# Kernel tuning notes

Hardware: AMD Instinct MI355X
Metric: run time of the kernel (lower is better)

The kernel has to match this reference:

```python
import jax, jax.numpy as jnp
import numpy as np

B, T, D_IN, D_OUT = 8, 2048, 4096, 4096
N_ADAPTERS, R_MAX = 8, 64


def setup_inputs() -> dict:
    key = jax.random.key(0)
    k_x, k_base, k_idx, k_A, k_B, k_s = jax.random.split(key, 6)
    x = jax.random.normal(k_x, (B, T, D_IN), dtype=jnp.float32)
    base_output = jax.random.normal(k_base, (B, T, D_OUT), dtype=jnp.float32)
    adapter_indices = jax.random.randint(k_idx, (B,), 0, N_ADAPTERS, dtype=jnp.int64)
    # He-uniform init for A (kaiming_uniform with a=sqrt(5) -> bound = 1/sqrt(fan_in))
    bound = 1.0 / np.sqrt(D_IN)
    lora_A = jax.random.uniform(k_A, (N_ADAPTERS, D_IN, R_MAX), dtype=jnp.float32,
                                minval=-bound, maxval=bound)
    # lora_B is zeros at init; use small random values for a non-trivial reference
    lora_B = jax.random.normal(k_B, (N_ADAPTERS, R_MAX, D_OUT), dtype=jnp.float32) * 0.02
    lora_scaling = jax.random.uniform(k_s, (N_ADAPTERS,), dtype=jnp.float32,
                                      minval=0.5, maxval=2.0)
    return {"x": x, "base_output": base_output, "adapter_indices": adapter_indices,
            "lora_A": lora_A, "lora_B": lora_B, "lora_scaling": lora_scaling}


def reference(x, base_output, adapter_indices, lora_A, lora_B, lora_scaling):
    # Gather per-batch adapter weights (adapter index broadcasts over sequence):
    # equivalent to sort-by-adapter -> grouped GEMM -> unsort, since every token
    # in a batch row shares one adapter and all ranks equal r_max.
    A_b = lora_A[adapter_indices]          # [B, D_IN, R]
    B_b = lora_B[adapter_indices]          # [B, R, D_OUT]
    s_b = lora_scaling[adapter_indices]    # [B]
    inter = jnp.einsum('btd,bdr->btr', x, A_b)        # [B, T, R]
    y = jnp.einsum('btr,bro->bto', inter, B_b)        # [B, T, D_OUT]
    return base_output + y * s_b[:, None, None]
```

## Files before the change

### kernel.cpp

```cpp
#include <hip/hip_runtime.h>
#include <hip/hip_bf16.h>
#include <cstdint>
#include <cstddef>

#define BT    16384
#define DIN   4096
#define DOUT  4096
#define RR    64
#define TSEQ  2048
#define NADP  8

typedef float  f32x4  __attribute__((ext_vector_type(4)));
typedef __bf16 bf16x8 __attribute__((ext_vector_type(8)));

static __device__ __forceinline__ unsigned short bf16_bits(float f) {
    return __builtin_bit_cast(unsigned short, (__bf16)f);
}

static __device__ __forceinline__ size_t i2_idx(int mblk, int rb, int mrow, int j) {
    return ((((size_t)mblk * 8 + rb) * 16 + mrow) * 8 + j);
}

__global__ __launch_bounds__(256) void k_prep_a(
    const float* __restrict__ A, __bf16* __restrict__ At2)
{
    const int gtid = blockIdx.x * 256 + threadIdx.x;
    const int r  = gtid & 63;
    const int kb = (gtid >> 6) & (DIN / 8 - 1);
    const int a  = gtid >> 15;
    const float* __restrict__ src = A + (size_t)a * DIN * RR + (size_t)kb * 8 * RR + r;
    unsigned int u[4];
    #pragma unroll
    for (int p = 0; p < 4; ++p) {
        unsigned int lo = bf16_bits(src[(2 * p + 0) * RR]);
        unsigned int hi = bf16_bits(src[(2 * p + 1) * RR]);
        u[p] = lo | (hi << 16);
    }
    *(uint4*)&At2[(size_t)gtid * 8] = make_uint4(u[0], u[1], u[2], u[3]);
}

__global__ __launch_bounds__(256) void k_prep_b(
    const float* __restrict__ Bw, __bf16* __restrict__ Bp)
{
    const int gtid = blockIdx.x * 256 + threadIdx.x;
    const int o  = gtid & (DOUT - 1);
    const int rb = (gtid >> 12) & 7;
    const int a  = gtid >> 15;
    const float* __restrict__ src = Bw + (size_t)a * RR * DOUT + (size_t)rb * 8 * DOUT + o;
    unsigned int u[4];
    #pragma unroll
    for (int p = 0; p < 4; ++p) {
        unsigned int lo = bf16_bits(src[(2 * p + 0) * DOUT]);
        unsigned int hi = bf16_bits(src[(2 * p + 1) * DOUT]);
        u[p] = lo | (hi << 16);
    }
    *(uint4*)&Bp[(size_t)gtid * 8] = make_uint4(u[0], u[1], u[2], u[3]);
}

static __device__ __forceinline__ bf16x8 cvt8(float4 a, float4 b) {
    bf16x8 v;
    v[0] = (__bf16)a.x; v[1] = (__bf16)a.y; v[2] = (__bf16)a.z; v[3] = (__bf16)a.w;
    v[4] = (__bf16)b.x; v[5] = (__bf16)b.y; v[6] = (__bf16)b.z; v[7] = (__bf16)b.w;
    return v;
}

__global__ __launch_bounds__(256, 2) void k_xa(
    const float* __restrict__ x, const int* __restrict__ idx,
    const __bf16* __restrict__ At2, __bf16* __restrict__ inter2)
{
    __shared__ __bf16 xs[2][32][64];

    const int tid  = threadIdx.x;
    const int m0   = blockIdx.x * 32;
    const int a    = idx[m0 / TSEQ];
    const int w    = tid >> 6, lane = tid & 63;
    const int mr   = lane & 15, kg = lane >> 4;

    const int srow = tid >> 3;
    const int sj   = tid & 7;
    const int sk8  = sj ^ (srow & 7);
    const float* __restrict__ xsrc = x + (size_t)(m0 + srow) * DIN + sk8 * 8;
    __bf16* const xdst0 = &xs[0][srow][sj * 8];
    __bf16* const xdst1 = &xs[1][srow][sj * 8];

    const __bf16* __restrict__ Aw = At2 + (size_t)a * RR * DIN;
    const int rcol = w * 16 + mr;

    f32x4 z = {0.f, 0.f, 0.f, 0.f};
    f32x4 acc0 = z, acc1 = z;

    float4 rbA0, rbA1, rbB0, rbB1;

    rbA0 = *(const float4*)(xsrc + 0 * 64);
    rbA1 = *(const float4*)(xsrc + 0 * 64 + 4);
    rbB0 = *(const float4*)(xsrc + 1 * 64);
    rbB1 = *(const float4*)(xsrc + 1 * 64 + 4);
    *(bf16x8*)xdst0 = cvt8(rbA0, rbA1);
    __syncthreads();

    for (int t2 = 0; t2 < 32; ++t2) {
        const int t = 2 * t2;
        const int tp2 = (t + 2 <= 63) ? (t + 2) : 63;
        const int tp3 = (t + 3 <= 63) ? (t + 3) : 63;

        rbA0 = *(const float4*)(xsrc + tp2 * 64);
        rbA1 = *(const float4*)(xsrc + tp2 * 64 + 4);
        #pragma unroll
        for (int kstep = 0; kstep < 2; ++kstep) {
            const int kq = kstep * 4 + kg;
            bf16x8 bfw = *(const bf16x8*)&Aw[((size_t)(t * 8 + kq) * 64 + rcol) * 8];
            bf16x8 af0 = *(const bf16x8*)&xs[0][mr]     [(kq ^ (mr & 7)) * 8];
            bf16x8 af1 = *(const bf16x8*)&xs[0][16 + mr][(kq ^ (mr & 7)) * 8];
            acc0 = __builtin_amdgcn_mfma_f32_16x16x32_bf16(af0, bfw, acc0, 0, 0, 0);
            acc1 = __builtin_amdgcn_mfma_f32_16x16x32_bf16(af1, bfw, acc1, 0, 0, 0);
        }
        *(bf16x8*)xdst1 = cvt8(rbB0, rbB1);
        __syncthreads();

        rbB0 = *(const float4*)(xsrc + tp3 * 64);
        rbB1 = *(const float4*)(xsrc + tp3 * 64 + 4);
        #pragma unroll
        for (int kstep = 0; kstep < 2; ++kstep) {
            const int kq = kstep * 4 + kg;
            bf16x8 bfw = *(const bf16x8*)&Aw[((size_t)((t + 1) * 8 + kq) * 64 + rcol) * 8];
            bf16x8 af0 = *(const bf16x8*)&xs[1][mr]     [(kq ^ (mr & 7)) * 8];
            bf16x8 af1 = *(const bf16x8*)&xs[1][16 + mr][(kq ^ (mr & 7)) * 8];
            acc0 = __builtin_amdgcn_mfma_f32_16x16x32_bf16(af0, bfw, acc0, 0, 0, 0);
            acc1 = __builtin_amdgcn_mfma_f32_16x16x32_bf16(af1, bfw, acc1, 0, 0, 0);
        }
        *(bf16x8*)xdst0 = cvt8(rbA0, rbA1);
        __syncthreads();
    }

    const int rb = w * 2 + (mr >> 3), j = mr & 7;
    #pragma unroll
    for (int q = 0; q < 4; ++q) {
        inter2[i2_idx(blockIdx.x * 2 + 0, rb, kg * 4 + q, j)] = (__bf16)acc0[q];
        inter2[i2_idx(blockIdx.x * 2 + 1, rb, kg * 4 + q, j)] = (__bf16)acc1[q];
    }
}

__global__ __launch_bounds__(256) void k_by(
    const __bf16* __restrict__ inter2, const float* __restrict__ base,
    const int* __restrict__ idx, const __bf16* __restrict__ Bp,
    const float* __restrict__ scal, float* __restrict__ out)
{
    const int o0 = blockIdx.x * 64;
    const int m0 = blockIdx.y * 64;
    const int a  = idx[m0 / TSEQ];
    const float s = scal[a];
    const __bf16* __restrict__ Ba = Bp + (size_t)a * RR * DOUT;
    const int lane = threadIdx.x & 63;
    const int w    = threadIdx.x >> 6;
    const int mr   = lane & 15, kg = lane >> 4;
    const int oc   = o0 + w * 16 + mr;

    f32x4 z = {0.f, 0.f, 0.f, 0.f};
    f32x4 acc[4] = {z, z, z, z};

    #pragma unroll
    for (int ksub = 0; ksub < 2; ++ksub) {
        const int rb = ksub * 4 + kg;
        bf16x8 bfA = *(const bf16x8*)&Ba[((size_t)rb * DOUT + oc) * 8];
        #pragma unroll
        for (int mt = 0; mt < 4; ++mt) {
            bf16x8 afB = *(const bf16x8*)&inter2[i2_idx(m0 / 16 + mt, rb, mr, 0)];
            acc[mt] = __builtin_amdgcn_mfma_f32_16x16x32_bf16(bfA, afB, acc[mt], 0, 0, 0);
        }
    }

    #pragma unroll
    for (int mt = 0; mt < 4; ++mt) {
        size_t off = (size_t)(m0 + mt * 16 + mr) * DOUT + o0 + w * 16 + kg * 4;
        float4 bv = *(const float4*)&base[off];
        float4 o;
        o.x = bv.x + s * acc[mt][0];
        o.y = bv.y + s * acc[mt][1];
        o.z = bv.z + s * acc[mt][2];
        o.w = bv.w + s * acc[mt][3];
        *(float4*)&out[off] = o;
    }
}

__global__ __launch_bounds__(256) void k_xa_fb(
    const float* __restrict__ x, const int* __restrict__ idx,
    const float* __restrict__ A, __bf16* __restrict__ inter)
{
    const int m0   = blockIdx.x * 32;
    const int a    = idx[m0 / TSEQ];
    const float* __restrict__ Aa = A + (size_t)a * DIN * RR;
    const int lane = threadIdx.x & 63;
    const int rw   = threadIdx.x >> 6;
    const int mr   = lane & 15, kg = lane >> 4;
    const int rcol = rw * 16 + mr;
    const float* __restrict__ xrow0 = x + (size_t)(m0 + mr) * DIN;
    const float* __restrict__ xrow1 = x + (size_t)(m0 + 16 + mr) * DIN;

    f32x4 acc0 = {0.f, 0.f, 0.f, 0.f};
    f32x4 acc1 = {0.f, 0.f, 0.f, 0.f};

    for (int k0 = 0; k0 < DIN; k0 += 64) {
        #pragma unroll
        for (int ksub = 0; ksub < 2; ++ksub) {
            const int koff = k0 + ksub * 32 + kg * 8;
            float4 u0 = *(const float4*)&xrow0[koff];
            float4 u1 = *(const float4*)&xrow0[koff + 4];
            float4 v0 = *(const float4*)&xrow1[koff];
            float4 v1 = *(const float4*)&xrow1[koff + 4];
            bf16x8 af0 = cvt8(u0, u1);
            bf16x8 af1 = cvt8(v0, v1);
            const float* ap = &Aa[(size_t)koff * RR + rcol];
            bf16x8 bf;
            bf[0] = (__bf16)ap[0 * RR]; bf[1] = (__bf16)ap[1 * RR];
            bf[2] = (__bf16)ap[2 * RR]; bf[3] = (__bf16)ap[3 * RR];
            bf[4] = (__bf16)ap[4 * RR]; bf[5] = (__bf16)ap[5 * RR];
            bf[6] = (__bf16)ap[6 * RR]; bf[7] = (__bf16)ap[7 * RR];
            acc0 = __builtin_amdgcn_mfma_f32_16x16x32_bf16(af0, bf, acc0, 0, 0, 0);
            acc1 = __builtin_amdgcn_mfma_f32_16x16x32_bf16(af1, bf, acc1, 0, 0, 0);
        }
    }
    #pragma unroll
    for (int q = 0; q < 4; ++q) {
        inter[(size_t)(m0 + kg * 4 + q) * RR + rcol]      = (__bf16)acc0[q];
        inter[(size_t)(m0 + 16 + kg * 4 + q) * RR + rcol] = (__bf16)acc1[q];
    }
}

__global__ __launch_bounds__(256) void k_by_fb(
    const __bf16* __restrict__ inter, const float* __restrict__ base,
    const int* __restrict__ idx, const float* __restrict__ Bw,
    const float* __restrict__ scal, float* __restrict__ out)
{
    const int o0 = blockIdx.x * 64;
    const int m0 = blockIdx.y * 64;
    const int a  = idx[m0 / TSEQ];
    const float s = scal[a];
    const float* __restrict__ Ba = Bw + (size_t)a * RR * DOUT;
    const int lane = threadIdx.x & 63;
    const int w    = threadIdx.x >> 6;
    const int mr   = lane & 15, kg = lane >> 4;
    const int oc   = o0 + w * 16 + mr;

    f32x4 z = {0.f, 0.f, 0.f, 0.f};
    f32x4 acc[4] = {z, z, z, z};

    #pragma unroll
    for (int ksub = 0; ksub < 2; ++ksub) {
        const int kb = ksub * 32 + kg * 8;
        const float* bp = &Ba[(size_t)kb * DOUT + oc];
        bf16x8 bf;
        bf[0] = (__bf16)bp[0 * DOUT]; bf[1] = (__bf16)bp[1 * DOUT];
        bf[2] = (__bf16)bp[2 * DOUT]; bf[3] = (__bf16)bp[3 * DOUT];
        bf[4] = (__bf16)bp[4 * DOUT]; bf[5] = (__bf16)bp[5 * DOUT];
        bf[6] = (__bf16)bp[6 * DOUT]; bf[7] = (__bf16)bp[7 * DOUT];
        #pragma unroll
        for (int mt = 0; mt < 4; ++mt) {
            bf16x8 af = *(const bf16x8*)&inter[(size_t)(m0 + mt * 16 + mr) * RR + kb];
            acc[mt] = __builtin_amdgcn_mfma_f32_16x16x32_bf16(af, bf, acc[mt], 0, 0, 0);
        }
    }
    #pragma unroll
    for (int mt = 0; mt < 4; ++mt) {
        #pragma unroll
        for (int q = 0; q < 4; ++q) {
            size_t off = (size_t)(m0 + mt * 16 + kg * 4 + q) * DOUT + oc;
            out[off] = base[off] + s * acc[mt][q];
        }
    }
}

extern "C" void kernel_launch(void* const* d_in, const int* in_sizes, int n_in,
                              void* d_out, int out_size, void* d_ws, size_t ws_size,
                              hipStream_t stream)
{
    const float* x    = (const float*)d_in[0];
    const float* base = (const float*)d_in[1];
    const int*   idx  = (const int*)  d_in[2];
    const float* A    = (const float*)d_in[3];
    const float* Bw   = (const float*)d_in[4];
    const float* scal = (const float*)d_in[5];
    float* out = (float*)d_out;

    const size_t INTER_B = (size_t)BT * RR * 2;
    const size_t AT_B    = (size_t)NADP * RR * DIN * 2;
    const size_t BT_B    = (size_t)NADP * DOUT * RR * 2;

    if (ws_size >= INTER_B + AT_B + BT_B) {
        __bf16* inter2 = (__bf16*)d_ws;
        __bf16* At2    = (__bf16*)((char*)d_ws + INTER_B);
        __bf16* Bp     = (__bf16*)((char*)d_ws + INTER_B + AT_B);
        k_prep_a<<<dim3(1024), 256, 0, stream>>>(A, At2);
        k_prep_b<<<dim3(1024), 256, 0, stream>>>(Bw, Bp);
        k_xa<<<dim3(BT / 32),            256, 0, stream>>>(x, idx, At2, inter2);
        k_by<<<dim3(DOUT / 64, BT / 64), 256, 0, stream>>>(inter2, base, idx, Bp, scal, out);
    } else {
        __bf16* inter = (__bf16*)d_ws;
        k_xa_fb<<<dim3(BT / 32),            256, 0, stream>>>(x, idx, A, inter);
        k_by_fb<<<dim3(DOUT / 64, BT / 64), 256, 0, stream>>>(inter, base, idx, Bw, scal, out);
    }
}
```

Before: 199.3 us.

## Stage fp32 x tiles via global_load_lds and convert to bf16 at fragment read

The x-times-A kernel now copies raw fp32 x tiles straight from global memory into LDS with direct global-to-LDS loads, using an XOR swizzle. The bf16 conversion moves to the point where MFMA fragments are read from LDS. This removes the register round trip and the explicit conversion before the shared-memory store, and makes the double-buffered pipeline one stage per iteration. In exchange the LDS footprint and LDS read traffic double, since tiles stay fp32, and every wave repeats the conversion work.

```diff
diff --git a/kernel.cpp b/kernel.cpp
--- a/kernel.cpp
+++ b/kernel.cpp
@@ -21,6 +21,28 @@
     return ((((size_t)mblk * 8 + rb) * 16 + mrow) * 8 + j);
 }
 
+static __device__ __forceinline__ bf16x8 cvt8(float4 a, float4 b) {
+    bf16x8 v;
+    v[0] = (__bf16)a.x; v[1] = (__bf16)a.y; v[2] = (__bf16)a.z; v[3] = (__bf16)a.w;
+    v[4] = (__bf16)b.x; v[5] = (__bf16)b.y; v[6] = (__bf16)b.z; v[7] = (__bf16)b.w;
+    return v;
+}
+
+static __device__ __forceinline__ bf16x8 cvt8v(f32x4 a, f32x4 b) {
+    bf16x8 v;
+    v[0] = (__bf16)a[0]; v[1] = (__bf16)a[1]; v[2] = (__bf16)a[2]; v[3] = (__bf16)a[3];
+    v[4] = (__bf16)b[0]; v[5] = (__bf16)b[1]; v[6] = (__bf16)b[2]; v[7] = (__bf16)b[3];
+    return v;
+}
+
+typedef const __attribute__((address_space(1))) void* gas1_t;
+typedef __attribute__((address_space(3))) void*       gas3_t;
+static __device__ __forceinline__ void gll16(const void* g, void* l) {
+    __builtin_amdgcn_global_load_lds((gas1_t)(uintptr_t)g,
+                                     (gas3_t)(uint32_t)(uintptr_t)l,
+                                     16, 0, 0);
+}
+
 __global__ __launch_bounds__(256) void k_prep_a(
     const float* __restrict__ A, __bf16* __restrict__ At2)
 {
@@ -57,80 +79,67 @@
     *(uint4*)&Bp[(size_t)gtid * 8] = make_uint4(u[0], u[1], u[2], u[3]);
 }
 
-static __device__ __forceinline__ bf16x8 cvt8(float4 a, float4 b) {
-    bf16x8 v;
-    v[0] = (__bf16)a.x; v[1] = (__bf16)a.y; v[2] = (__bf16)a.z; v[3] = (__bf16)a.w;
-    v[4] = (__bf16)b.x; v[5] = (__bf16)b.y; v[6] = (__bf16)b.z; v[7] = (__bf16)b.w;
-    return v;
-}
-
 __global__ __launch_bounds__(256, 2) void k_xa(
     const float* __restrict__ x, const int* __restrict__ idx,
     const __bf16* __restrict__ At2, __bf16* __restrict__ inter2)
 {
-    __shared__ __bf16 xs[2][32][64];
-
-    const int tid  = threadIdx.x;
+    __shared__ float xs[2][32][64];
+
     const int m0   = blockIdx.x * 32;
     const int a    = idx[m0 / TSEQ];
-    const int w    = tid >> 6, lane = tid & 63;
+    const int w    = threadIdx.x >> 6, lane = threadIdx.x & 63;
     const int mr   = lane & 15, kg = lane >> 4;
-
-    const int srow = tid >> 3;
-    const int sj   = tid & 7;
-    const int sk8  = sj ^ (srow & 7);
-    const float* __restrict__ xsrc = x + (size_t)(m0 + srow) * DIN + sk8 * 8;
-    __bf16* const xdst0 = &xs[0][srow][sj * 8];
-    __bf16* const xdst1 = &xs[1][srow][sj * 8];
+    const int rcol = w * 16 + mr;
 
     const __bf16* __restrict__ Aw = At2 + (size_t)a * RR * DIN;
-    const int rcol = w * 16 + mr;
+
+    const float* gsrc0;
+    const float* gsrc1;
+    {
+        const int R0 = w * 8 + 0 * 4 + kg;
+        const int R1 = w * 8 + 1 * 4 + kg;
+        const int s0 = (lane & 15) ^ (R0 & 15);
+        const int s1 = (lane & 15) ^ (R1 & 15);
+        gsrc0 = x + (size_t)(m0 + R0) * DIN + s0 * 4;
+        gsrc1 = x + (size_t)(m0 + R1) * DIN + s1 * 4;
+    }
 
     f32x4 z = {0.f, 0.f, 0.f, 0.f};
     f32x4 acc0 = z, acc1 = z;
 
-    float4 rbA0, rbA1, rbB0, rbB1;
-
-    rbA0 = *(const float4*)(xsrc + 0 * 64);
-    rbA1 = *(const float4*)(xsrc + 0 * 64 + 4);
-    rbB0 = *(const float4*)(xsrc + 1 * 64);
-    rbB1 = *(const float4*)(xsrc + 1 * 64 + 4);
-    *(bf16x8*)xdst0 = cvt8(rbA0, rbA1);
+#define STAGE(B, T)                                                      \
+    {                                                                    \
+        gll16(gsrc0 + (T) * 64, &xs[B][w * 8 + 0][0]);                   \
+        gll16(gsrc1 + (T) * 64, &xs[B][w * 8 + 4][0]);                   \
+    }
+
+#define COMPUTE(B, T)                                                              \
+    {                                                                              \
+        _Pragma("unroll")                                                          \
+        for (int ksub = 0; ksub < 2; ++ksub) {                                     \
+            const int kq = ksub * 4 + kg;                                          \
+            bf16x8 bfw = *(const bf16x8*)&Aw[(((size_t)(T) * 8 + kq) * 64 + rcol) * 8]; \
+            f32x4 lo0 = *(const f32x4*)&xs[B][mr]     [((2 * kq)     ^ mr) * 4];   \
+            f32x4 hi0 = *(const f32x4*)&xs[B][mr]     [((2 * kq + 1) ^ mr) * 4];   \
+            f32x4 lo1 = *(const f32x4*)&xs[B][16 + mr][((2 * kq)     ^ mr) * 4];   \
+            f32x4 hi1 = *(const f32x4*)&xs[B][16 + mr][((2 * kq + 1) ^ mr) * 4];   \
+            acc0 = __builtin_amdgcn_mfma_f32_16x16x32_bf16(cvt8v(lo0, hi0), bfw, acc0, 0, 0, 0); \
+            acc1 = __builtin_amdgcn_mfma_f32_16x16x32_bf16(cvt8v(lo1, hi1), bfw, acc1, 0, 0, 0); \
+        }                                                                          \
+    }
+
+    STAGE(0, 0)
     __syncthreads();
 
-    for (int t2 = 0; t2 < 32; ++t2) {
-        const int t = 2 * t2;
-        const int tp2 = (t + 2 <= 63) ? (t + 2) : 63;
-        const int tp3 = (t + 3 <= 63) ? (t + 3) : 63;
-
-        rbA0 = *(const float4*)(xsrc + tp2 * 64);
-        rbA1 = *(const float4*)(xsrc + tp2 * 64 + 4);
-        #pragma unroll
-        for (int kstep = 0; kstep < 2; ++kstep) {
-            const int kq = kstep * 4 + kg;
-            bf16x8 bfw = *(const bf16x8*)&Aw[((size_t)(t * 8 + kq) * 64 + rcol) * 8];
-            bf16x8 af0 = *(const bf16x8*)&xs[0][mr]     [(kq ^ (mr & 7)) * 8];
-            bf16x8 af1 = *(const bf16x8*)&xs[0][16 + mr][(kq ^ (mr & 7)) * 8];
-            acc0 = __builtin_amdgcn_mfma_f32_16x16x32_bf16(af0, bfw, acc0, 0, 0, 0);
-            acc1 = __builtin_amdgcn_mfma_f32_16x16x32_bf16(af1, bfw, acc1, 0, 0, 0);
-        }
-        *(bf16x8*)xdst1 = cvt8(rbB0, rbB1);
+    for (int t = 0; t < 63; ++t) {
+        STAGE((t + 1) & 1, t + 1)
+        COMPUTE(t & 1, t)
         __syncthreads();
-
-        rbB0 = *(const float4*)(xsrc + tp3 * 64);
-        rbB1 = *(const float4*)(xsrc + tp3 * 64 + 4);
-        #pragma unroll
-        for (int kstep = 0; kstep < 2; ++kstep) {
-            const int kq = kstep * 4 + kg;
-            bf16x8 bfw = *(const bf16x8*)&Aw[((size_t)((t + 1) * 8 + kq) * 64 + rcol) * 8];
-            bf16x8 af0 = *(const bf16x8*)&xs[1][mr]     [(kq ^ (mr & 7)) * 8];
-            bf16x8 af1 = *(const bf16x8*)&xs[1][16 + mr][(kq ^ (mr & 7)) * 8];
-            acc0 = __builtin_amdgcn_mfma_f32_16x16x32_bf16(af0, bfw, acc0, 0, 0, 0);
-            acc1 = __builtin_amdgcn_mfma_f32_16x16x32_bf16(af1, bfw, acc1, 0, 0, 0);
-        }
-        *(bf16x8*)xdst0 = cvt8(rbA0, rbA1);
-        __syncthreads();
-    }
+    }
+    COMPUTE(1, 63)
+
+#undef STAGE
+#undef COMPUTE
 
     const int rb = w * 2 + (mr >> 3), j = mr & 7;
     #pragma unroll
```

Result: slower. 206.8 us (+3.8%).
